# Performance work log

Hardware: AMD Instinct MI355X
Metric: run time of the kernel (lower is better)

Reference implementation:

```python
import jax, jax.numpy as jnp
import numpy as np

B = 131072
RES_DIM = 100
N_CHAMBERS = 6
CF_ITERS = 5
CF_K = 0.02

COUPLING = np.array([
    [0.0, -0.3, 0.6, 0.4, -0.2, 0.3],
    [-0.3, 0.0, -0.5, -0.7, 0.6, 0.4],
    [0.6, -0.5, 0.0, 0.3, -0.3, 0.2],
    [0.4, -0.7, 0.3, 0.0, -0.4, 0.5],
    [-0.2, 0.6, -0.3, -0.4, 0.0, 0.3],
    [0.3, 0.4, 0.2, 0.5, 0.3, 0.0],
], dtype=np.float32)
DECAY = np.array([0.9, 0.93, 0.85, 0.97, 0.88, 0.94], dtype=np.float32)


def setup_inputs() -> dict:
    key = jax.random.key(0)
    ks = jax.random.split(key, 9)
    def lin(k, fan_in, fan_out):
        kw, kb = jax.random.split(k)
        bound = 1.0 / np.sqrt(fan_in)
        W = jax.random.uniform(kw, (N_CHAMBERS, fan_in, fan_out), jnp.float32, -bound, bound)
        b = jax.random.uniform(kb, (N_CHAMBERS, fan_out), jnp.float32, -bound, bound)
        return W, b
    W1, b1 = lin(ks[0], RES_DIM, 128)
    W2, b2 = lin(ks[1], 128, 64)
    W3, b3 = lin(ks[2], 64, 32)
    W4, b4 = lin(ks[3], 32, 1)
    W4 = W4[:, :, 0]  # (6, 32)
    b4 = b4[:, 0]     # (6,)
    res = jax.random.normal(ks[4], (B, RES_DIM), jnp.float32)
    return {
        "res": res,
        "W1": W1, "b1": b1, "W2": W2, "b2": b2,
        "W3": W3, "b3": b3, "W4": W4, "b4": b4,
        "coupling": jnp.asarray(COUPLING),
        "decay": jnp.asarray(DECAY),
    }


def reference(res, W1, b1, W2, b2, W3, b3, W4, b4, coupling, decay):
    # 6 per-chamber MLP towers, batched over the chamber axis c.
    h = jax.nn.silu(jnp.einsum('bd,cdh->cbh', res, W1) + b1[:, None, :])   # (6,B,128)
    h = jax.nn.silu(jnp.einsum('cbh,cho->cbo', h, W2) + b2[:, None, :])    # (6,B,64)
    h = jax.nn.silu(jnp.einsum('cbh,cho->cbo', h, W3) + b3[:, None, :])    # (6,B,32)
    raw = (jnp.einsum('cbh,ch->cb', h, W4) + b4[:, None]).T                # (B,6)
    # 5-step coupled sigmoid recurrence on the tiny (B,6) state.
    act = jax.nn.sigmoid(raw)
    for _ in range(CF_ITERS):
        delta = ((act * decay) @ coupling) * CF_K
        act = jax.nn.sigmoid(raw + delta)
    return act, raw
```

## Files before the change

### kernel.cpp

```cpp
#include <hip/hip_runtime.h>
#include <hip/hip_bf16.h>
#include <stdint.h>

#define B_TOTAL 131072

typedef __attribute__((ext_vector_type(8))) short short8;
typedef __attribute__((ext_vector_type(16))) float float16v;
typedef __attribute__((ext_vector_type(2))) float f32x2;

#define CH_U16 24576
#define oF2 14336
#define oF3 22528
#define BF16_TOT (6 * CH_U16)
#define F32_BASE (BF16_TOT / 2)
#define sB1 0
#define sB2 768
#define sB3 1152
#define sW4 1344
#define sB4 1536
#define sCP 1542
#define sDC 1578
#define NSMALL 1584
#define CONV_TOT (BF16_TOT + NSMALL)

#define GLB_AS __attribute__((address_space(1)))
#define LDS_AS __attribute__((address_space(3)))

__device__ __forceinline__ float bf16_as_f32(uint16_t u) {
    union { uint32_t i; float f; } v; v.i = ((uint32_t)u) << 16; return v.f;
}
__device__ __forceinline__ uint16_t f2bf(float f) {
    uint32_t u = __float_as_uint(f);
    return (uint16_t)((u + 0x7FFFu + ((u >> 16) & 1u)) >> 16);
}
__device__ __forceinline__ float sigmoidf_fast(float x) {
    return __builtin_amdgcn_rcpf(1.0f + __expf(-x));
}
__device__ __forceinline__ float siluf(float x) { return x * sigmoidf_fast(x); }

__device__ __forceinline__ float readsrc(const void* p, int off, bool bf) {
    return bf ? bf16_as_f32(((const uint16_t*)p)[off]) : ((const float*)p)[off];
}

__device__ __forceinline__ uint32_t cvtpk_bf16(float lo, float hi) {
    uint32_t r;
    asm("v_cvt_pk_bf16_f32 %0, %1, %2" : "=v"(r) : "v"(lo), "v"(hi));
    return r;
}

__device__ __forceinline__ uint32_t silu2bf(float a, float b) {
    float ea = __expf(-a), eb = __expf(-b);
    f32x2 e; e.x = ea; e.y = eb;
    f32x2 one; one.x = 1.0f; one.y = 1.0f;
    f32x2 d = e + one;
    float p = d.x * d.y;
    float rp = __builtin_amdgcn_rcpf(p);
    f32x2 s; s.x = d.y * rp; s.y = d.x * rp;
    f32x2 x; x.x = a; x.y = b;
    f32x2 o = x * s;
    return cvtpk_bf16(o.x, o.y);
}

__global__ void convert_kernel(const void* W1, const void* b1, const void* W2, const void* b2,
                               const void* W3, const void* b3, const void* W4, const void* b4,
                               const void* cp, const void* dc, uint16_t* __restrict__ wsb) {
    const bool bf = (((const uint32_t*)cp)[0] != 0u);
    int idx = blockIdx.x * 256 + threadIdx.x;
    if (idx >= CONV_TOT) return;
    if (idx < BF16_TOT) {
        int c = idx / CH_U16;
        int r = idx - c * CH_U16;
        float v;
        if (r < oF2) {
            int f = r >> 9, rem = r & 511, l = rem >> 3, e = rem & 7;
            int ct = f / 7, kb = f - ct * 7;
            int n = ct * 32 + (l & 31), k = kb * 16 + (l >> 5) * 8 + e;
            v = (k < 100) ? readsrc(W1, c * 12800 + k * 128 + n, bf) : 0.0f;
        } else if (r < oF3) {
            int j = r - oF2;
            int f = j >> 9, rem = j & 511, l = rem >> 3, e = rem & 7;
            int ct2 = f >> 3, kb = f & 7;
            int n = ct2 * 32 + (l & 31);
            int k = 32 * (kb >> 1) + 8 * (e >> 1) + 4 * (l >> 5) + 2 * (kb & 1) + (e & 1);
            v = readsrc(W2, c * 8192 + k * 64 + n, bf);
        } else {
            int j = r - oF3;
            int kb = j >> 9, rem = j & 511, l = rem >> 3, e = rem & 7;
            int n = (l & 31);
            int k = 32 * (kb >> 1) + 8 * (e >> 1) + 4 * (l >> 5) + 2 * (kb & 1) + (e & 1);
            v = readsrc(W3, c * 2048 + k * 32 + n, bf);
        }
        wsb[idx] = f2bf(v);
    } else {
        int fi = idx - BF16_TOT;
        float v;
        if      (fi < sB2)  v = readsrc(b1, fi, bf);
        else if (fi < sB3)  v = readsrc(b2, fi - sB2, bf);
        else if (fi < sW4)  v = readsrc(b3, fi - sB3, bf);
        else if (fi < sB4)  v = readsrc(W4, fi - sW4, bf);
        else if (fi < sCP)  v = readsrc(b4, fi - sB4, bf);
        else if (fi < sDC)  v = readsrc(cp, fi - sCP, bf);
        else                v = readsrc(dc, fi - sDC, bf);
        ((float*)wsb)[F32_BASE + fi] = v;
    }
}

union Frag { uint4 u4; uint2 u2[2]; uint32_t u[4]; short8 s8; uint16_t h[8]; };

__global__ __launch_bounds__(512, 4)
void chambers_mfma(const void* __restrict__ resv, const uint16_t* __restrict__ wsb,
                   const uint32_t* __restrict__ cpw, float* __restrict__ outF) {
    const float* wsf = (const float*)wsb;
    const bool bfin = (cpw[0] != 0u);
    const int tid = threadIdx.x;
    const int w = tid >> 6, l = tid & 63;
    const int l5 = l & 31, q2 = l >> 5;
    const int row = blockIdx.x * 256 + w * 32 + l5;

    __shared__ __align__(16) uint16_t sW[CH_U16];
    __shared__ __align__(16) float sB[NSMALL];

#define STAGE(CC)                                                              \
    {                                                                          \
        const uint16_t* gsrc = wsb + (CC) * CH_U16;                            \
        _Pragma("unroll")                                                      \
        for (int rr = 0; rr < 6; ++rr) {                                       \
            const int i = rr * 8 + w;                   \
            __builtin_amdgcn_global_load_lds(                                  \
                (const GLB_AS uint32_t*)(gsrc + i * 512 + l * 8),              \
                (LDS_AS uint32_t*)(sW + i * 512), 16, 0, 0);                   \
        }                                                                      \
    }

    STAGE(0)
    for (int i = tid; i < NSMALL; i += 512) sB[i] = wsf[F32_BASE + i];

    Frag R[7];
    if (bfin) {
        const uint16_t* bp = (const uint16_t*)resv + (size_t)row * 100;
#pragma unroll
        for (int kb = 0; kb < 6; ++kb) {
            const int k0 = kb * 16 + q2 * 8;
            R[kb].u2[0] = *(const uint2*)(bp + k0);
            R[kb].u2[1] = *(const uint2*)(bp + k0 + 4);
        }
        R[6].u4 = make_uint4(0, 0, 0, 0);
        if (q2 == 0) R[6].u2[0] = *(const uint2*)(bp + 96);
    } else {
        const float* fp = (const float*)resv + (size_t)row * 100;
#pragma unroll
        for (int kb = 0; kb < 6; ++kb) {
            const int k0 = kb * 16 + q2 * 8;
            float4 x0 = *(const float4*)(fp + k0);
            float4 x1 = *(const float4*)(fp + k0 + 4);
            R[kb].u[0] = cvtpk_bf16(x0.x, x0.y);
            R[kb].u[1] = cvtpk_bf16(x0.z, x0.w);
            R[kb].u[2] = cvtpk_bf16(x1.x, x1.y);
            R[kb].u[3] = cvtpk_bf16(x1.z, x1.w);
        }
        R[6].u4 = make_uint4(0, 0, 0, 0);
        if (q2 == 0) {
            float4 x0 = *(const float4*)(fp + 96);
            R[6].u[0] = cvtpk_bf16(x0.x, x0.y);
            R[6].u[1] = cvtpk_bf16(x0.z, x0.w);
        }
    }

    __syncthreads();

    float raw0 = 0.f, raw1 = 0.f, raw2 = 0.f, raw3 = 0.f, raw4 = 0.f, raw5 = 0.f;
    Frag pk1f[2][4];
    Frag pk2f[2][2];

#pragma unroll 1
    for (int c = 0; c < 6; ++c) {
#pragma unroll
        for (int ct = 0; ct < 4; ++ct) {
            float16v acc;
#pragma unroll
            for (int ar = 0; ar < 4; ++ar) {
                const float4 bv = *(const float4*)(sB + sB1 + c * 128 + ct * 32 + ar * 8 + q2 * 4);
                acc[4 * ar + 0] = bv.x; acc[4 * ar + 1] = bv.y;
                acc[4 * ar + 2] = bv.z; acc[4 * ar + 3] = bv.w;
            }
            const uint16_t* fp1 = sW + (ct * 7) * 512 + l * 8;
#pragma unroll
            for (int kb = 0; kb < 7; ++kb) {
                Frag Af; Af.u4 = *(const uint4*)(fp1 + kb * 512);
                acc = __builtin_amdgcn_mfma_f32_32x32x16_bf16(Af.s8, R[kb].s8, acc, 0, 0, 0);
            }
#pragma unroll
            for (int ar = 0; ar < 4; ++ar) {
                pk1f[0][ct].u[ar] = silu2bf(acc[4 * ar + 0], acc[4 * ar + 1]);
                pk1f[1][ct].u[ar] = silu2bf(acc[4 * ar + 2], acc[4 * ar + 3]);
            }
        }

#pragma unroll
        for (int ct2 = 0; ct2 < 2; ++ct2) {
            float16v acc;
#pragma unroll
            for (int ar = 0; ar < 4; ++ar) {
                const float4 bv = *(const float4*)(sB + sB2 + c * 64 + ct2 * 32 + ar * 8 + q2 * 4);
                acc[4 * ar + 0] = bv.x; acc[4 * ar + 1] = bv.y;
                acc[4 * ar + 2] = bv.z; acc[4 * ar + 3] = bv.w;
            }
            const uint16_t* fp2 = sW + oF2 + (ct2 * 8) * 512 + l * 8;
#pragma unroll
            for (int kb = 0; kb < 8; ++kb) {
                Frag Af; Af.u4 = *(const uint4*)(fp2 + kb * 512);
                acc = __builtin_amdgcn_mfma_f32_32x32x16_bf16(Af.s8, pk1f[kb & 1][kb >> 1].s8, acc, 0, 0, 0);
            }
#pragma unroll
            for (int ar = 0; ar < 4; ++ar) {
                pk2f[0][ct2].u[ar] = silu2bf(acc[4 * ar + 0], acc[4 * ar + 1]);
                pk2f[1][ct2].u[ar] = silu2bf(acc[4 * ar + 2], acc[4 * ar + 3]);
            }
        }

        {
            float16v acc;
#pragma unroll
            for (int ar = 0; ar < 4; ++ar) {
                const float4 bv = *(const float4*)(sB + sB3 + c * 32 + ar * 8 + q2 * 4);
                acc[4 * ar + 0] = bv.x; acc[4 * ar + 1] = bv.y;
                acc[4 * ar + 2] = bv.z; acc[4 * ar + 3] = bv.w;
            }
            const uint16_t* fp3 = sW + oF3 + l * 8;
#pragma unroll
            for (int kb = 0; kb < 4; ++kb) {
                Frag Af; Af.u4 = *(const uint4*)(fp3 + kb * 512);
                acc = __builtin_amdgcn_mfma_f32_32x32x16_bf16(Af.s8, pk2f[kb & 1][kb >> 1].s8, acc, 0, 0, 0);
            }
            float part = 0.f;
#pragma unroll
            for (int ar = 0; ar < 4; ++ar) {
                const float4 wv = *(const float4*)(sB + sW4 + c * 32 + ar * 8 + q2 * 4);
                part = fmaf(siluf(acc[4 * ar + 0]), wv.x, part);
                part = fmaf(siluf(acc[4 * ar + 1]), wv.y, part);
                part = fmaf(siluf(acc[4 * ar + 2]), wv.z, part);
                part = fmaf(siluf(acc[4 * ar + 3]), wv.w, part);
            }
            part += __shfl_xor(part, 32);
            const float rv = part + sB[sB4 + c];
            raw0 = (c == 0) ? rv : raw0;
            raw1 = (c == 1) ? rv : raw1;
            raw2 = (c == 2) ? rv : raw2;
            raw3 = (c == 3) ? rv : raw3;
            raw4 = (c == 4) ? rv : raw4;
            raw5 = (c == 5) ? rv : raw5;
        }

        if (c < 5) {
            __syncthreads();
            STAGE(c + 1)
            __syncthreads();
        }
    }

    const float rv6[6] = {raw0, raw1, raw2, raw3, raw4, raw5};
    float av[6];
#pragma unroll
    for (int c = 0; c < 6; ++c) av[c] = sigmoidf_fast(rv6[c]);
    const float K = 0.02f;
#pragma unroll 1
    for (int it = 0; it < 5; ++it) {
        float tt[6];
#pragma unroll
        for (int i = 0; i < 6; ++i) tt[i] = av[i] * sB[sDC + i] * K;
#pragma unroll
        for (int j = 0; j < 6; ++j) {
            float dl = 0.0f;
#pragma unroll
            for (int i = 0; i < 6; ++i) dl = fmaf(tt[i], sB[sCP + i * 6 + j], dl);
            av[j] = sigmoidf_fast(rv6[j] + dl);
        }
    }
    if (q2 == 0) {
        float2* oa = (float2*)(outF + (size_t)row * 6);
        oa[0] = make_float2(av[0], av[1]);
        oa[1] = make_float2(av[2], av[3]);
        oa[2] = make_float2(av[4], av[5]);
        float2* orw = (float2*)(outF + (size_t)B_TOTAL * 6 + (size_t)row * 6);
        orw[0] = make_float2(rv6[0], rv6[1]);
        orw[1] = make_float2(rv6[2], rv6[3]);
        orw[2] = make_float2(rv6[4], rv6[5]);
    }
#undef STAGE
}

extern "C" void kernel_launch(void* const* d_in, const int* in_sizes, int n_in,
                              void* d_out, int out_size, void* d_ws, size_t ws_size,
                              hipStream_t stream) {
    uint16_t* wsb = (uint16_t*)d_ws;
    convert_kernel<<<(CONV_TOT + 255) / 256, 256, 0, stream>>>(
        d_in[1], d_in[2], d_in[3], d_in[4], d_in[5], d_in[6], d_in[7], d_in[8],
        d_in[9], d_in[10], wsb);
    chambers_mfma<<<B_TOTAL / 256, 512, 0, stream>>>(
        d_in[0], wsb, (const uint32_t*)d_in[9], (float*)d_out);
}
```

Measured before the change: 160.1 us.

## Interleave two chamber towers per pass and read layer-2 weights from global

```diff
diff --git a/kernel.cpp b/kernel.cpp
--- a/kernel.cpp
+++ b/kernel.cpp
@@ -22,6 +22,9 @@
 #define sDC 1578
 #define NSMALL 1584
 #define CONV_TOT (BF16_TOT + NSMALL)
+
+#define bWF3 14336
+#define BUFC 16384
 
 #define GLB_AS __attribute__((address_space(1)))
 #define LDS_AS __attribute__((address_space(3)))
@@ -107,6 +110,89 @@
 
 union Frag { uint4 u4; uint2 u2[2]; uint32_t u[4]; short8 s8; uint16_t h[8]; };
 
+struct ChSt {
+    float16v acc;
+    Frag pk1f[2][4];
+    Frag pk2f[2][2];
+    const uint16_t* buf;
+    const uint16_t* gF2;
+    int c;
+};
+
+template<int T>
+__device__ __forceinline__ void MF(ChSt& st, const float* sB, const Frag* R,
+                                   int q2, int l) {
+    if constexpr (T < 4) {
+#pragma unroll
+        for (int ar = 0; ar < 4; ++ar) {
+            const float4 bv = *(const float4*)(sB + sB1 + st.c * 128 + T * 32 + ar * 8 + q2 * 4);
+            st.acc[4 * ar + 0] = bv.x; st.acc[4 * ar + 1] = bv.y;
+            st.acc[4 * ar + 2] = bv.z; st.acc[4 * ar + 3] = bv.w;
+        }
+        const uint16_t* fp1 = st.buf + (T * 7) * 512 + l * 8;
+#pragma unroll
+        for (int kb = 0; kb < 7; ++kb) {
+            Frag Af; Af.u4 = *(const uint4*)(fp1 + kb * 512);
+            st.acc = __builtin_amdgcn_mfma_f32_32x32x16_bf16(Af.s8, R[kb].s8, st.acc, 0, 0, 0);
+        }
+    } else if constexpr (T < 6) {
+        const int ct2 = T - 4;
+#pragma unroll
+        for (int ar = 0; ar < 4; ++ar) {
+            const float4 bv = *(const float4*)(sB + sB2 + st.c * 64 + ct2 * 32 + ar * 8 + q2 * 4);
+            st.acc[4 * ar + 0] = bv.x; st.acc[4 * ar + 1] = bv.y;
+            st.acc[4 * ar + 2] = bv.z; st.acc[4 * ar + 3] = bv.w;
+        }
+#pragma unroll
+        for (int kb = 0; kb < 8; ++kb) {
+            Frag Af; Af.u4 = *(const uint4*)(st.gF2 + ((ct2 * 8 + kb) * 64 + l) * 8);
+            st.acc = __builtin_amdgcn_mfma_f32_32x32x16_bf16(Af.s8, st.pk1f[kb & 1][kb >> 1].s8, st.acc, 0, 0, 0);
+        }
+    } else {
+#pragma unroll
+        for (int ar = 0; ar < 4; ++ar) {
+            const float4 bv = *(const float4*)(sB + sB3 + st.c * 32 + ar * 8 + q2 * 4);
+            st.acc[4 * ar + 0] = bv.x; st.acc[4 * ar + 1] = bv.y;
+            st.acc[4 * ar + 2] = bv.z; st.acc[4 * ar + 3] = bv.w;
+        }
+        const uint16_t* fp3 = st.buf + bWF3 + l * 8;
+#pragma unroll
+        for (int kb = 0; kb < 4; ++kb) {
+            Frag Af; Af.u4 = *(const uint4*)(fp3 + kb * 512);
+            st.acc = __builtin_amdgcn_mfma_f32_32x32x16_bf16(Af.s8, st.pk2f[kb & 1][kb >> 1].s8, st.acc, 0, 0, 0);
+        }
+    }
+}
+
+template<int T>
+__device__ __forceinline__ void SL(ChSt& st, const float* sB, int q2, float& rv) {
+    if constexpr (T < 4) {
+#pragma unroll
+        for (int ar = 0; ar < 4; ++ar) {
+            st.pk1f[0][T].u[ar] = silu2bf(st.acc[4 * ar + 0], st.acc[4 * ar + 1]);
+            st.pk1f[1][T].u[ar] = silu2bf(st.acc[4 * ar + 2], st.acc[4 * ar + 3]);
+        }
+    } else if constexpr (T < 6) {
+#pragma unroll
+        for (int ar = 0; ar < 4; ++ar) {
+            st.pk2f[0][T - 4].u[ar] = silu2bf(st.acc[4 * ar + 0], st.acc[4 * ar + 1]);
+            st.pk2f[1][T - 4].u[ar] = silu2bf(st.acc[4 * ar + 2], st.acc[4 * ar + 3]);
+        }
+    } else {
+        float part = 0.f;
+#pragma unroll
+        for (int ar = 0; ar < 4; ++ar) {
+            const float4 wv = *(const float4*)(sB + sW4 + st.c * 32 + ar * 8 + q2 * 4);
+            part = fmaf(siluf(st.acc[4 * ar + 0]), wv.x, part);
+            part = fmaf(siluf(st.acc[4 * ar + 1]), wv.y, part);
+            part = fmaf(siluf(st.acc[4 * ar + 2]), wv.z, part);
+            part = fmaf(siluf(st.acc[4 * ar + 3]), wv.w, part);
+        }
+        part += __shfl_xor(part, 32);
+        rv = part + sB[sB4 + st.c];
+    }
+}
+
 __global__ __launch_bounds__(512, 4)
 void chambers_mfma(const void* __restrict__ resv, const uint16_t* __restrict__ wsb,
                    const uint32_t* __restrict__ cpw, float* __restrict__ outF) {
@@ -117,22 +203,27 @@
     const int l5 = l & 31, q2 = l >> 5;
     const int row = blockIdx.x * 256 + w * 32 + l5;
 
-    __shared__ __align__(16) uint16_t sW[CH_U16];
+    __shared__ __align__(16) uint16_t sW[2 * BUFC];
     __shared__ __align__(16) float sB[NSMALL];
 
-#define STAGE(CC)                                                              \
+#define STAGE_PAIR(P)                                                          \
     {                                                                          \
-        const uint16_t* gsrc = wsb + (CC) * CH_U16;                            \
         _Pragma("unroll")                                                      \
-        for (int rr = 0; rr < 6; ++rr) {                                       \
-            const int i = rr * 8 + w;                   \
-            __builtin_amdgcn_global_load_lds(                                  \
-                (const GLB_AS uint32_t*)(gsrc + i * 512 + l * 8),              \
-                (LDS_AS uint32_t*)(sW + i * 512), 16, 0, 0);                   \
+        for (int sl = 0; sl < 2; ++sl) {                                       \
+            const uint16_t* gsrc = wsb + (2 * (P) + sl) * CH_U16;              \
+            uint16_t* ldst = sW + sl * BUFC;                                   \
+            _Pragma("unroll")                                                  \
+            for (int rr = 0; rr < 4; ++rr) {                                   \
+                const int i = rr * 8 + w;                     \
+                const int gi = (i < 28) ? i : (i + 16);                        \
+                __builtin_amdgcn_global_load_lds(                              \
+                    (const GLB_AS uint32_t*)(gsrc + gi * 512 + l * 8),         \
+                    (LDS_AS uint32_t*)(ldst + i * 512), 16, 0, 0);             \
+            }                                                                  \
         }                                                                      \
     }
 
-    STAGE(0)
+    STAGE_PAIR(0)
     for (int i = tid; i < NSMALL; i += 512) sB[i] = wsf[F32_BASE + i];
 
     Frag R[7];
@@ -169,91 +260,41 @@
     __syncthreads();
 
     float raw0 = 0.f, raw1 = 0.f, raw2 = 0.f, raw3 = 0.f, raw4 = 0.f, raw5 = 0.f;
-    Frag pk1f[2][4];
-    Frag pk2f[2][2];
+    ChSt A, B;
 
 #pragma unroll 1
-    for (int c = 0; c < 6; ++c) {
-#pragma unroll
-        for (int ct = 0; ct < 4; ++ct) {
-            float16v acc;
-#pragma unroll
-            for (int ar = 0; ar < 4; ++ar) {
-                const float4 bv = *(const float4*)(sB + sB1 + c * 128 + ct * 32 + ar * 8 + q2 * 4);
-                acc[4 * ar + 0] = bv.x; acc[4 * ar + 1] = bv.y;
-                acc[4 * ar + 2] = bv.z; acc[4 * ar + 3] = bv.w;
-            }
-            const uint16_t* fp1 = sW + (ct * 7) * 512 + l * 8;
-#pragma unroll
-            for (int kb = 0; kb < 7; ++kb) {
-                Frag Af; Af.u4 = *(const uint4*)(fp1 + kb * 512);
-                acc = __builtin_amdgcn_mfma_f32_32x32x16_bf16(Af.s8, R[kb].s8, acc, 0, 0, 0);
-            }
-#pragma unroll
-            for (int ar = 0; ar < 4; ++ar) {
-                pk1f[0][ct].u[ar] = silu2bf(acc[4 * ar + 0], acc[4 * ar + 1]);
-                pk1f[1][ct].u[ar] = silu2bf(acc[4 * ar + 2], acc[4 * ar + 3]);
-            }
-        }
-
-#pragma unroll
-        for (int ct2 = 0; ct2 < 2; ++ct2) {
-            float16v acc;
-#pragma unroll
-            for (int ar = 0; ar < 4; ++ar) {
-                const float4 bv = *(const float4*)(sB + sB2 + c * 64 + ct2 * 32 + ar * 8 + q2 * 4);
-                acc[4 * ar + 0] = bv.x; acc[4 * ar + 1] = bv.y;
-                acc[4 * ar + 2] = bv.z; acc[4 * ar + 3] = bv.w;
-            }
-            const uint16_t* fp2 = sW + oF2 + (ct2 * 8) * 512 + l * 8;
-#pragma unroll
-            for (int kb = 0; kb < 8; ++kb) {
-                Frag Af; Af.u4 = *(const uint4*)(fp2 + kb * 512);
-                acc = __builtin_amdgcn_mfma_f32_32x32x16_bf16(Af.s8, pk1f[kb & 1][kb >> 1].s8, acc, 0, 0, 0);
-            }
-#pragma unroll
-            for (int ar = 0; ar < 4; ++ar) {
-                pk2f[0][ct2].u[ar] = silu2bf(acc[4 * ar + 0], acc[4 * ar + 1]);
-                pk2f[1][ct2].u[ar] = silu2bf(acc[4 * ar + 2], acc[4 * ar + 3]);
-            }
-        }
-
-        {
-            float16v acc;
-#pragma unroll
-            for (int ar = 0; ar < 4; ++ar) {
-                const float4 bv = *(const float4*)(sB + sB3 + c * 32 + ar * 8 + q2 * 4);
-                acc[4 * ar + 0] = bv.x; acc[4 * ar + 1] = bv.y;
-                acc[4 * ar + 2] = bv.z; acc[4 * ar + 3] = bv.w;
-            }
-            const uint16_t* fp3 = sW + oF3 + l * 8;
-#pragma unroll
-            for (int kb = 0; kb < 4; ++kb) {
-                Frag Af; Af.u4 = *(const uint4*)(fp3 + kb * 512);
-                acc = __builtin_amdgcn_mfma_f32_32x32x16_bf16(Af.s8, pk2f[kb & 1][kb >> 1].s8, acc, 0, 0, 0);
-            }
-            float part = 0.f;
-#pragma unroll
-            for (int ar = 0; ar < 4; ++ar) {
-                const float4 wv = *(const float4*)(sB + sW4 + c * 32 + ar * 8 + q2 * 4);
-                part = fmaf(siluf(acc[4 * ar + 0]), wv.x, part);
-                part = fmaf(siluf(acc[4 * ar + 1]), wv.y, part);
-                part = fmaf(siluf(acc[4 * ar + 2]), wv.z, part);
-                part = fmaf(siluf(acc[4 * ar + 3]), wv.w, part);
-            }
-            part += __shfl_xor(part, 32);
-            const float rv = part + sB[sB4 + c];
-            raw0 = (c == 0) ? rv : raw0;
-            raw1 = (c == 1) ? rv : raw1;
-            raw2 = (c == 2) ? rv : raw2;
-            raw3 = (c == 3) ? rv : raw3;
-            raw4 = (c == 4) ? rv : raw4;
-            raw5 = (c == 5) ? rv : raw5;
-        }
-
-        if (c < 5) {
+    for (int p = 0; p < 3; ++p) {
+        const int cA = 2 * p, cB = 2 * p + 1;
+        A.c = cA; A.buf = sW;        A.gF2 = wsb + cA * CH_U16 + oF2;
+        B.c = cB; B.buf = sW + BUFC; B.gF2 = wsb + cB * CH_U16 + oF2;
+        float rvA = 0.f, rvB = 0.f;
+
+        MF<0>(A, sB, R, q2, l);
+        MF<0>(B, sB, R, q2, l);  SL<0>(A, sB, q2, rvA);
+        MF<1>(A, sB, R, q2, l);  SL<0>(B, sB, q2, rvB);
+        MF<1>(B, sB, R, q2, l);  SL<1>(A, sB, q2, rvA);
+        MF<2>(A, sB, R, q2, l);  SL<1>(B, sB, q2, rvB);
+        MF<2>(B, sB, R, q2, l);  SL<2>(A, sB, q2, rvA);
+        MF<3>(A, sB, R, q2, l);  SL<2>(B, sB, q2, rvB);
+        MF<3>(B, sB, R, q2, l);  SL<3>(A, sB, q2, rvA);
+        MF<4>(A, sB, R, q2, l);  SL<3>(B, sB, q2, rvB);
+        MF<4>(B, sB, R, q2, l);  SL<4>(A, sB, q2, rvA);
+        MF<5>(A, sB, R, q2, l);  SL<4>(B, sB, q2, rvB);
+        MF<5>(B, sB, R, q2, l);  SL<5>(A, sB, q2, rvA);
+        MF<6>(A, sB, R, q2, l);  SL<5>(B, sB, q2, rvB);
+        MF<6>(B, sB, R, q2, l);  SL<6>(A, sB, q2, rvA);
+        SL<6>(B, sB, q2, rvB);
+
+        raw0 = (cA == 0) ? rvA : raw0;
+        raw2 = (cA == 2) ? rvA : raw2;
+        raw4 = (cA == 4) ? rvA : raw4;
+        raw1 = (cB == 1) ? rvB : raw1;
+        raw3 = (cB == 3) ? rvB : raw3;
+        raw5 = (cB == 5) ? rvB : raw5;
+
+        if (p < 2) {
             __syncthreads();
-            STAGE(c + 1)
+            STAGE_PAIR(p + 1)
             __syncthreads();
         }
     }
@@ -286,7 +327,7 @@
         orw[1] = make_float2(rv6[2], rv6[3]);
         orw[2] = make_float2(rv6[4], rv6[5]);
     }
-#undef STAGE
+#undef STAGE_PAIR
 }
 
 extern "C" void kernel_launch(void* const* d_in, const int* in_sizes, int n_in,
```

After: 186.6 us. 1.17x slower.
